# Kernel optimization log

Measured on AMD Instinct MI355X. Metric: run time of the kernel, lower is better.

The kernel has to match this reference:

```python
import jax, jax.numpy as jnp
import numpy as np

MARGIN = 0.2


def colbert_score(q, d):
    # q: (B, Q, D), d: (B, K, D) -> scalar
    sim = jnp.einsum('bqd,bkd->bqk', q, d)          # (B, Q, K)
    max_sim = jnp.max(sim, axis=2)                   # (B, Q) row-wise max over doc tokens
    return jnp.sum(max_sim)                          # sum over query tokens and batch


def setup_inputs() -> dict:
    key = jax.random.key(0)
    k1, k2, k3 = jax.random.split(key, 3)
    B, Q, K, D = 256, 256, 512, 128
    return {
        'q': jax.random.normal(k1, (B, Q, D), dtype=jnp.float32),
        'p': jax.random.normal(k2, (B, K, D), dtype=jnp.float32),
        'n': jax.random.normal(k3, (B, K, D), dtype=jnp.float32),
    }


def reference(q, p, n):
    pos_score = colbert_score(q, p)
    neg_score = colbert_score(q, n)
    loss = jax.nn.relu(MARGIN + neg_score - pos_score)
    # torch .mean() on a scalar is identity
    return loss
```

## Files before the change

### kernel.cpp

```cpp
#include <hip/hip_runtime.h>


#define MARGIN   0.2f
#define Bn       256
#define Qn       256
#define Kn       512
#define Dn       128
#define TN       32
#define NT       (Kn / TN)
#define BSTR     136
#define NTHREADS 256

typedef __attribute__((ext_vector_type(8))) short short8;
typedef __attribute__((ext_vector_type(4))) short short4v;
typedef __attribute__((ext_vector_type(4))) float f32x4;

__device__ __forceinline__ void split_trunc(float x, unsigned short& hi, unsigned short& lo) {
    unsigned int u = __float_as_uint(x);
    hi = (unsigned short)(u >> 16);
    float l = x - __uint_as_float(u & 0xFFFF0000u);
    lo = (unsigned short)(__float_as_uint(l) >> 16);
}

__global__ __launch_bounds__(NTHREADS, 2)
void colbert_pass_kernel(const float* __restrict__ qg,
                         const float* __restrict__ pg,
                         const float* __restrict__ ng,
                         double* __restrict__ sum_ws) {
    __shared__ short Bs[2][2][TN * BSTR];
    __shared__ float part[4];

    const int tid  = threadIdx.x;
    const int w    = tid >> 6;
    const int lane = tid & 63;
    const int l16  = lane & 15;
    const int quad = lane >> 4;
    const int b    = blockIdx.x;
    const int pass = blockIdx.y;

    const float* docb = (pass ? ng : pg) + (size_t)b * Kn * Dn;

    float4 pre[4];
    {
        const float4* s4 = (const float4*)docb;
#pragma unroll
        for (int k = 0; k < 4; ++k) pre[k] = s4[tid + 256 * k];
    }

    short8 Ahi[4][4], Alo[4][4];
    {
        const float* qb = qg + (size_t)b * Qn * Dn;
#pragma unroll
        for (int mi = 0; mi < 4; ++mi)
#pragma unroll
            for (int ks = 0; ks < 4; ++ks) {
                const float* src = qb + (size_t)(w * 64 + mi * 16 + l16) * Dn
                                      + ks * 32 + quad * 8;
                float4 v0 = *(const float4*)src;
                float4 v1 = *(const float4*)(src + 4);
                float x[8] = {v0.x, v0.y, v0.z, v0.w, v1.x, v1.y, v1.z, v1.w};
#pragma unroll
                for (int j = 0; j < 8; ++j) {
                    unsigned short h, l;
                    split_trunc(x[j], h, l);
                    Ahi[mi][ks][j] = (short)h;
                    Alo[mi][ks][j] = (short)l;
                }
            }
    }

    float maxv[4][4];
#pragma unroll
    for (int mi = 0; mi < 4; ++mi)
#pragma unroll
        for (int r = 0; r < 4; ++r) maxv[mi][r] = -3e38f;

    int buf = 0;
    for (int t = 0; t < NT; ++t) {
#pragma unroll
        for (int k = 0; k < 4; ++k) {
            int i   = tid + 256 * k;
            int doc = i >> 5;
            int d4  = i & 31;
            float4 v = pre[k];
            float x[4] = {v.x, v.y, v.z, v.w};
            short4v hi, lo;
#pragma unroll
            for (int j = 0; j < 4; ++j) {
                unsigned short h, l;
                split_trunc(x[j], h, l);
                hi[j] = (short)h;
                lo[j] = (short)l;
            }
            *(short4v*)&Bs[buf][0][doc * BSTR + d4 * 4] = hi;
            *(short4v*)&Bs[buf][1][doc * BSTR + d4 * 4] = lo;
        }
        __syncthreads();

        if (t + 1 < NT) {
            const float4* s4 = (const float4*)(docb + (size_t)(t + 1) * TN * Dn);
#pragma unroll
            for (int k = 0; k < 4; ++k) pre[k] = s4[tid + 256 * k];
        }

        f32x4 acc[4][2];
#pragma unroll
        for (int mi = 0; mi < 4; ++mi)
#pragma unroll
            for (int ni = 0; ni < 2; ++ni) acc[mi][ni] = (f32x4){0.f, 0.f, 0.f, 0.f};

#pragma unroll
        for (int ni = 0; ni < 2; ++ni) {
            short8 bhi[4], blo[4];
#pragma unroll
            for (int ks = 0; ks < 4; ++ks) {
                int off = (ni * 16 + l16) * BSTR + ks * 32 + quad * 8;
                bhi[ks] = *(const short8*)&Bs[buf][0][off];
                blo[ks] = *(const short8*)&Bs[buf][1][off];
            }
#pragma unroll
            for (int ks = 0; ks < 4; ++ks) {
#pragma unroll
                for (int mi = 0; mi < 4; ++mi)
                    acc[mi][ni] = __builtin_amdgcn_mfma_f32_16x16x32_bf16(
                        Ahi[mi][ks], bhi[ks], acc[mi][ni], 0, 0, 0);
#pragma unroll
                for (int mi = 0; mi < 4; ++mi)
                    acc[mi][ni] = __builtin_amdgcn_mfma_f32_16x16x32_bf16(
                        Alo[mi][ks], bhi[ks], acc[mi][ni], 0, 0, 0);
#pragma unroll
                for (int mi = 0; mi < 4; ++mi)
                    acc[mi][ni] = __builtin_amdgcn_mfma_f32_16x16x32_bf16(
                        Ahi[mi][ks], blo[ks], acc[mi][ni], 0, 0, 0);
            }
        }

#pragma unroll
        for (int mi = 0; mi < 4; ++mi)
#pragma unroll
            for (int r = 0; r < 4; ++r)
                maxv[mi][r] = fmaxf(maxv[mi][r], fmaxf(acc[mi][0][r], acc[mi][1][r]));
        buf ^= 1;
    }

#pragma unroll
    for (int off = 1; off < 16; off <<= 1)
#pragma unroll
        for (int mi = 0; mi < 4; ++mi)
#pragma unroll
            for (int r = 0; r < 4; ++r)
                maxv[mi][r] = fmaxf(maxv[mi][r], __shfl_xor(maxv[mi][r], off));

    float s = 0.f;
#pragma unroll
    for (int mi = 0; mi < 4; ++mi)
#pragma unroll
        for (int r = 0; r < 4; ++r) s += maxv[mi][r];
    if (l16 != 0) s = 0.f;
    s += __shfl_xor(s, 16);
    s += __shfl_xor(s, 32);
    if (lane == 0) part[w] = s;
    __syncthreads();
    if (tid == 0) {
        double t = (double)part[0] + part[1] + part[2] + part[3];
        atomicAdd(sum_ws, pass ? -t : t);
    }
}

__global__ void finalize_kernel(const double* __restrict__ sum_ws,
                                float* __restrict__ out) {
    out[0] = fmaxf(0.0f, MARGIN - (float)sum_ws[0]);
}

extern "C" void kernel_launch(void* const* d_in, const int* in_sizes, int n_in,
                              void* d_out, int out_size, void* d_ws, size_t ws_size,
                              hipStream_t stream) {
    const float* q = (const float*)d_in[0];
    const float* p = (const float*)d_in[1];
    const float* n = (const float*)d_in[2];
    float* out = (float*)d_out;
    double* ws = (double*)d_ws;

    hipMemsetAsync(ws, 0, sizeof(double), stream);

    colbert_pass_kernel<<<dim3(Bn, 2), NTHREADS, 0, stream>>>(q, p, n, ws);
    finalize_kernel<<<1, 1, 0, stream>>>(ws, out);
}
```

Baseline: 180.3 us.

## Split query rows across two blocks to raise occupancy and grid size

Adds a grid z-dimension that splits the 256 query rows into two halves, so each wave holds 32 query rows of hi/lo bf16 fragments instead of 64. Launch bounds rise to 4 blocks per CU and B fragments are loaded per k-step rather than batched, cutting register pressure. This aims to improve latency hiding and fill more CUs. In exchange, each doc tile is fetched from global memory and converted to bf16 hi/lo twice, and there is less MFMA work per LDS load.

```diff
diff --git a/kernel.cpp b/kernel.cpp
--- a/kernel.cpp
+++ b/kernel.cpp
@@ -10,6 +10,7 @@
 #define NT       (Kn / TN)
 #define BSTR     136
 #define NTHREADS 256
+#define MI       2
 
 typedef __attribute__((ext_vector_type(8))) short short8;
 typedef __attribute__((ext_vector_type(4))) short short4v;
@@ -22,11 +23,11 @@
     lo = (unsigned short)(__float_as_uint(l) >> 16);
 }
 
-__global__ __launch_bounds__(NTHREADS, 2)
-void colbert_pass_kernel(const float* __restrict__ qg,
-                         const float* __restrict__ pg,
-                         const float* __restrict__ ng,
-                         double* __restrict__ sum_ws) {
+__global__ __launch_bounds__(NTHREADS, 4)
+void colbert_q4_kernel(const float* __restrict__ qg,
+                       const float* __restrict__ pg,
+                       const float* __restrict__ ng,
+                       double* __restrict__ sum_ws) {
     __shared__ short Bs[2][2][TN * BSTR];
     __shared__ float part[4];
 
@@ -37,6 +38,7 @@
     const int quad = lane >> 4;
     const int b    = blockIdx.x;
     const int pass = blockIdx.y;
+    const int qh   = blockIdx.z;
 
     const float* docb = (pass ? ng : pg) + (size_t)b * Kn * Dn;
 
@@ -47,14 +49,14 @@
         for (int k = 0; k < 4; ++k) pre[k] = s4[tid + 256 * k];
     }
 
-    short8 Ahi[4][4], Alo[4][4];
+    short8 Ahi[MI][4], Alo[MI][4];
     {
-        const float* qb = qg + (size_t)b * Qn * Dn;
+        const float* qb = qg + ((size_t)b * Qn + qh * 128) * Dn;
 #pragma unroll
-        for (int mi = 0; mi < 4; ++mi)
+        for (int mi = 0; mi < MI; ++mi)
 #pragma unroll
             for (int ks = 0; ks < 4; ++ks) {
-                const float* src = qb + (size_t)(w * 64 + mi * 16 + l16) * Dn
+                const float* src = qb + (size_t)(w * 32 + mi * 16 + l16) * Dn
                                       + ks * 32 + quad * 8;
                 float4 v0 = *(const float4*)src;
                 float4 v1 = *(const float4*)(src + 4);
@@ -69,9 +71,9 @@
             }
     }
 
-    float maxv[4][4];
+    float maxv[MI][4];
 #pragma unroll
-    for (int mi = 0; mi < 4; ++mi)
+    for (int mi = 0; mi < MI; ++mi)
 #pragma unroll
         for (int r = 0; r < 4; ++r) maxv[mi][r] = -3e38f;
 
@@ -103,40 +105,36 @@
             for (int k = 0; k < 4; ++k) pre[k] = s4[tid + 256 * k];
         }
 
-        f32x4 acc[4][2];
+        f32x4 acc[MI][2];
 #pragma unroll
-        for (int mi = 0; mi < 4; ++mi)
+        for (int mi = 0; mi < MI; ++mi)
 #pragma unroll
             for (int ni = 0; ni < 2; ++ni) acc[mi][ni] = (f32x4){0.f, 0.f, 0.f, 0.f};
 
 #pragma unroll
         for (int ni = 0; ni < 2; ++ni) {
-            short8 bhi[4], blo[4];
 #pragma unroll
             for (int ks = 0; ks < 4; ++ks) {
                 int off = (ni * 16 + l16) * BSTR + ks * 32 + quad * 8;
-                bhi[ks] = *(const short8*)&Bs[buf][0][off];
-                blo[ks] = *(const short8*)&Bs[buf][1][off];
-            }
+                short8 bhi = *(const short8*)&Bs[buf][0][off];
+                short8 blo = *(const short8*)&Bs[buf][1][off];
 #pragma unroll
-            for (int ks = 0; ks < 4; ++ks) {
+                for (int mi = 0; mi < MI; ++mi)
+                    acc[mi][ni] = __builtin_amdgcn_mfma_f32_16x16x32_bf16(
+                        Ahi[mi][ks], bhi, acc[mi][ni], 0, 0, 0);
 #pragma unroll
-                for (int mi = 0; mi < 4; ++mi)
+                for (int mi = 0; mi < MI; ++mi)
                     acc[mi][ni] = __builtin_amdgcn_mfma_f32_16x16x32_bf16(
-                        Ahi[mi][ks], bhi[ks], acc[mi][ni], 0, 0, 0);
+                        Alo[mi][ks], bhi, acc[mi][ni], 0, 0, 0);
 #pragma unroll
-                for (int mi = 0; mi < 4; ++mi)
+                for (int mi = 0; mi < MI; ++mi)
                     acc[mi][ni] = __builtin_amdgcn_mfma_f32_16x16x32_bf16(
-                        Alo[mi][ks], bhi[ks], acc[mi][ni], 0, 0, 0);
-#pragma unroll
-                for (int mi = 0; mi < 4; ++mi)
-                    acc[mi][ni] = __builtin_amdgcn_mfma_f32_16x16x32_bf16(
-                        Ahi[mi][ks], blo[ks], acc[mi][ni], 0, 0, 0);
+                        Ahi[mi][ks], blo, acc[mi][ni], 0, 0, 0);
             }
         }
 
 #pragma unroll
-        for (int mi = 0; mi < 4; ++mi)
+        for (int mi = 0; mi < MI; ++mi)
 #pragma unroll
             for (int r = 0; r < 4; ++r)
                 maxv[mi][r] = fmaxf(maxv[mi][r], fmaxf(acc[mi][0][r], acc[mi][1][r]));
@@ -146,14 +144,14 @@
 #pragma unroll
     for (int off = 1; off < 16; off <<= 1)
 #pragma unroll
-        for (int mi = 0; mi < 4; ++mi)
+        for (int mi = 0; mi < MI; ++mi)
 #pragma unroll
             for (int r = 0; r < 4; ++r)
                 maxv[mi][r] = fmaxf(maxv[mi][r], __shfl_xor(maxv[mi][r], off));
 
     float s = 0.f;
 #pragma unroll
-    for (int mi = 0; mi < 4; ++mi)
+    for (int mi = 0; mi < MI; ++mi)
 #pragma unroll
         for (int r = 0; r < 4; ++r) s += maxv[mi][r];
     if (l16 != 0) s = 0.f;
@@ -183,6 +181,6 @@
 
     hipMemsetAsync(ws, 0, sizeof(double), stream);
 
-    colbert_pass_kernel<<<dim3(Bn, 2), NTHREADS, 0, stream>>>(q, p, n, ws);
+    colbert_q4_kernel<<<dim3(Bn, 2, 2), NTHREADS, 0, stream>>>(q, p, n, ws);
     finalize_kernel<<<1, 1, 0, stream>>>(ws, out);
 }
```

Result: no change. 183.1 us (+1.6%).
